# Performance work log

Measured on AMD Instinct MI355X. Metric: run time of the kernel, lower is better.

Reference implementation:

```python
import jax, jax.numpy as jnp
import numpy as np

BLANK = 0  # matches GreedyCTCDecoder(blank=0)


def setup_inputs() -> dict:
    key = jax.random.key(0)
    T, V = 65536, 512  # [num_seq, num_label]
    emission = jax.random.normal(key, (T, V), dtype=jnp.float32)
    return {"emission": emission}


def reference(emission):
    """Greedy CTC decode, array form of GreedyCTCDecoder.forward.

    The original does a per-timestep argmax (with a host sync every step),
    maps blank -> ' ' and non-blank index i -> labels[i-1 if i > 1 else 0],
    then collapses consecutive duplicates. Here we compute:
      index : [T] argmax label id per timestep (the tensor the module returns)
      keep  : [T] bool mask marking the timesteps that survive the
              blank/repeat collapse (i.e. the characters of `final`).
    """
    index = jnp.argmax(emission, axis=-1)  # [T]
    # character id actually emitted per step (original's quirky mapping):
    #   blank -> -1 (stands for the ' ' that gets stripped/collapsed)
    #   i > 1 -> i - 1 ; i == 1 -> 0
    char = jnp.where(index == BLANK, -1, jnp.where(index > 1, index - 1, 0))
    # collapse consecutive repeats; drop blanks (the strip/' ' removal)
    prev = jnp.concatenate([jnp.full((1,), -2, dtype=char.dtype), char[:-1]])
    keep = (char != prev) & (char != -1)
    return (index, keep)
```

## Files before the change

### kernel.cpp

```cpp
#include <hip/hip_runtime.h>
#include <hip/hip_bf16.h>


#define T_ROWS 65536
#define V_LABELS 512

__global__ __launch_bounds__(256) void ctc_argmax_kernel(
    const float* __restrict__ em, int* __restrict__ out_idx) {
    const int wave = (blockIdx.x * blockDim.x + threadIdx.x) >> 6;
    const int lane = threadIdx.x & 63;
    if (wave >= T_ROWS) return;

    const float4* row = reinterpret_cast<const float4*>(
        em + (size_t)wave * V_LABELS);

    float4 a = row[lane];
    float4 b = row[lane + 64];

    float bv = a.x;
    int bi = 4 * lane;
    if (a.y > bv) { bv = a.y; bi = 4 * lane + 1; }
    if (a.z > bv) { bv = a.z; bi = 4 * lane + 2; }
    if (a.w > bv) { bv = a.w; bi = 4 * lane + 3; }
    if (b.x > bv) { bv = b.x; bi = 256 + 4 * lane; }
    if (b.y > bv) { bv = b.y; bi = 256 + 4 * lane + 1; }
    if (b.z > bv) { bv = b.z; bi = 256 + 4 * lane + 2; }
    if (b.w > bv) { bv = b.w; bi = 256 + 4 * lane + 3; }

    #pragma unroll
    for (int m = 1; m < 64; m <<= 1) {
        float ov = __shfl_xor(bv, m, 64);
        int   oi = __shfl_xor(bi, m, 64);
        if (ov > bv || (ov == bv && oi < bi)) { bv = ov; bi = oi; }
    }

    if (lane == 0) out_idx[wave] = bi;
}

__global__ __launch_bounds__(256) void ctc_keep_kernel(
    const int* __restrict__ idx, int* __restrict__ keep) {
    const int t = blockIdx.x * blockDim.x + threadIdx.x;
    if (t >= T_ROWS) return;
    const int cur = idx[t];
    bool k;
    if (t == 0) {
        k = (cur != 0);
    } else {
        const int prev = idx[t - 1];
        k = (cur != 0) && (cur != prev);
    }
    keep[t] = k ? 1 : 0;
}

extern "C" void kernel_launch(void* const* d_in, const int* in_sizes, int n_in,
                              void* d_out, int out_size, void* d_ws, size_t ws_size,
                              hipStream_t stream) {
    const float* em = (const float*)d_in[0];
    int* out = (int*)d_out;
    int* out_idx  = out;
    int* out_keep = out + T_ROWS;

    const int waves_per_block = 256 / 64;
    const int grid_argmax = T_ROWS / waves_per_block;
    ctc_argmax_kernel<<<grid_argmax, 256, 0, stream>>>(em, out_idx);

    const int grid_keep = (T_ROWS + 255) / 256;
    ctc_keep_kernel<<<grid_keep, 256, 0, stream>>>(out_idx, out_keep);
}
```

Measured before the change: 184.1 us.

## Fuse argmax and keep into one kernel with multiple rows per wave

Merges the argmax and keep-mask kernels into one launch. Each wave now handles 8 rows, and the previous-row index is passed between waves through shared memory. Each block recomputes the argmax of the row just before it to get its boundary value. This removes the second launch and the idx round trip to memory, and gives each wave more loads in flight. The cost is one redundant row read per block, a block-wide sync, and fewer blocks in the grid.

```diff
diff --git a/kernel.cpp b/kernel.cpp
--- a/kernel.cpp
+++ b/kernel.cpp
@@ -1,21 +1,19 @@
 #include <hip/hip_runtime.h>
-#include <hip/hip_bf16.h>
 
 
 #define T_ROWS 65536
 #define V_LABELS 512
+#define RPW 8
+#define WPB 4
+#define RPB (RPW * WPB)
+#define NBLOCKS (T_ROWS / RPB)
 
-__global__ __launch_bounds__(256) void ctc_argmax_kernel(
-    const float* __restrict__ em, int* __restrict__ out_idx) {
-    const int wave = (blockIdx.x * blockDim.x + threadIdx.x) >> 6;
-    const int lane = threadIdx.x & 63;
-    if (wave >= T_ROWS) return;
-
-    const float4* row = reinterpret_cast<const float4*>(
-        em + (size_t)wave * V_LABELS);
-
-    float4 a = row[lane];
-    float4 b = row[lane + 64];
+__device__ __forceinline__ int argmax_row(const float* __restrict__ em,
+                                          int row, int lane) {
+    const float4* rp =
+        reinterpret_cast<const float4*>(em + (size_t)row * V_LABELS);
+    float4 a = rp[lane];
+    float4 b = rp[lane + 64];
 
     float bv = a.x;
     int bi = 4 * lane;
@@ -33,23 +31,49 @@
         int   oi = __shfl_xor(bi, m, 64);
         if (ov > bv || (ov == bv && oi < bi)) { bv = ov; bi = oi; }
     }
-
-    if (lane == 0) out_idx[wave] = bi;
+    return bi;
 }
 
-__global__ __launch_bounds__(256) void ctc_keep_kernel(
-    const int* __restrict__ idx, int* __restrict__ keep) {
-    const int t = blockIdx.x * blockDim.x + threadIdx.x;
-    if (t >= T_ROWS) return;
-    const int cur = idx[t];
-    bool k;
-    if (t == 0) {
-        k = (cur != 0);
-    } else {
-        const int prev = idx[t - 1];
-        k = (cur != 0) && (cur != prev);
+__global__ __launch_bounds__(256) void ctc_fused_kernel(
+    const float* __restrict__ em, int* __restrict__ out_idx,
+    int* __restrict__ out_keep) {
+    const int lane = threadIdx.x & 63;
+    const int w    = threadIdx.x >> 6;
+    const int blockBase = blockIdx.x * RPB;
+    const int waveBase  = blockBase + w * RPW;
+
+    __shared__ int s_last[WPB];
+    __shared__ int s_prevblock;
+
+    int prevIdx = -2;
+    if (w == 0 && blockIdx.x > 0)
+        prevIdx = argmax_row(em, blockBase - 1, lane);
+
+    int idxs[RPW];
+    #pragma unroll
+    for (int r = 0; r < RPW; ++r)
+        idxs[r] = argmax_row(em, waveBase + r, lane);
+
+    if (lane == 0) {
+        s_last[w] = idxs[RPW - 1];
+        if (w == 0) s_prevblock = prevIdx;
     }
-    keep[t] = k ? 1 : 0;
+    __syncthreads();
+
+    int prev = (w > 0) ? s_last[w - 1] : s_prevblock;
+
+    int my_idx = 0, my_keep = 0;
+    #pragma unroll
+    for (int r = 0; r < RPW; ++r) {
+        const int cur = idxs[r];
+        const int k   = (cur != 0 && cur != prev) ? 1 : 0;
+        if (lane == r) { my_idx = cur; my_keep = k; }
+        prev = cur;
+    }
+    if (lane < RPW) {
+        out_idx[waveBase + lane]  = my_idx;
+        out_keep[waveBase + lane] = my_keep;
+    }
 }
 
 extern "C" void kernel_launch(void* const* d_in, const int* in_sizes, int n_in,
@@ -57,13 +81,5 @@
                               hipStream_t stream) {
     const float* em = (const float*)d_in[0];
     int* out = (int*)d_out;
-    int* out_idx  = out;
-    int* out_keep = out + T_ROWS;
-
-    const int waves_per_block = 256 / 64;
-    const int grid_argmax = T_ROWS / waves_per_block;
-    ctc_argmax_kernel<<<grid_argmax, 256, 0, stream>>>(em, out_idx);
-
-    const int grid_keep = (T_ROWS + 255) / 256;
-    ctc_keep_kernel<<<grid_keep, 256, 0, stream>>>(out_idx, out_keep);
+    ctc_fused_kernel<<<NBLOCKS, 256, 0, stream>>>(em, out, out + T_ROWS);
 }
```

Result: slower. 190.8 us (+3.6%).
